# Optimization experiments

Measured on AMD Instinct MI355X. Metric: run time of the kernel, lower is better.

## Reference

```python
import jax, jax.numpy as jnp
import numpy as np

EPS = 1e-8

def _center(G):
    # Double-centering: H @ G @ H with H = I - 11^T/n, expressed as mean subtraction.
    # Identical math to the torch H-matmul version, O(n^2) instead of O(n^3).
    row = jnp.mean(G, axis=-1, keepdims=True)
    col = jnp.mean(G, axis=-2, keepdims=True)
    tot = jnp.mean(G, axis=(-2, -1), keepdims=True)
    return G - row - col + tot


def setup_inputs() -> dict:
    key = jax.random.key(0)
    k1, k2 = jax.random.split(key)
    B, L, H, M = 32, 128, 512, 512
    x = jax.random.normal(k1, (B, L, H), dtype=jnp.float32)
    # nn.Embedding.from_pretrained(torch.normal(-0.01, 0.2, (M, L*H)))
    centroid_w = jax.random.normal(k2, (M, L * H), dtype=jnp.float32) * 0.2 - 0.01
    return {"x": x, "centroid_w": centroid_w}


def reference(x, centroid_w):
    B, L, H = x.shape
    M = centroid_w.shape[0]
    cent = centroid_w.reshape(M, L, H)

    # Centered linear Grams
    Cx = _center(jnp.einsum('blh,bkh->blk', x, x))        # (B, L, L)
    Cy = _center(jnp.einsum('mlh,mkh->mlk', cent, cent))  # (M, L, L)

    # linear HSIC: sum over LxL of elementwise product -> (B, M)
    hsic = jnp.einsum('bij,mij->bm', Cx, Cy)
    vx = jnp.sqrt(jnp.sum(Cx * Cx, axis=(1, 2)))  # (B,)  sqrt(HSIC(x,x))
    vy = jnp.sqrt(jnp.sum(Cy * Cy, axis=(1, 2)))  # (M,)  sqrt(HSIC(y,y))
    cka_loss_matrix = -jnp.log(jnp.abs(hsic / (vx[:, None] * vy[None, :])) + EPS)

    idx = jnp.argmax(cka_loss_matrix, axis=-1)  # (B,)
    sel = cent[idx]                              # (B, L, H) gathered centroids

    # Second CKA pass against selected centroids; torch broadcasting makes (B, B)
    Cs = _center(jnp.einsum('blh,bkh->blk', sel, sel))  # (B, L, L)
    hsic2 = jnp.einsum('bij,cij->bc', Cx, Cs)           # (B, B)
    vs = jnp.sqrt(jnp.sum(Cs * Cs, axis=(1, 2)))        # (B,)
    cka_loss = -jnp.log(jnp.mean(jnp.abs(hsic2 / (vx[:, None] * vs[None, :]))) + EPS)

    return cka_loss, cka_loss_matrix, idx
```

## Files before the change

### kernel.cpp

```cpp
#include <hip/hip_runtime.h>
#include <math.h>

#define BB 32
#define LL 128
#define HH 512
#define MM 512
#define NM 544
#define EPSF 1e-8f
#define CPLEN 9216
#define NCH 36

typedef __attribute__((ext_vector_type(8))) short short8b;
typedef __attribute__((ext_vector_type(4))) float f32x4;

#define NWS_CP     0
#define NWS_PART   5013504
#define NWS_NSQ    5603328
#define NWS_HSIC   5603872
#define NWS_IDS    5620256

__device__ __forceinline__ float4 shflx1(float4 a) {
    float4 r;
    r.x = __shfl_xor(a.x, 1, 64);
    r.y = __shfl_xor(a.y, 1, 64);
    r.z = __shfl_xor(a.z, 1, 64);
    r.w = __shfl_xor(a.w, 1, 64);
    return r;
}

__device__ __forceinline__ unsigned pack2(unsigned lo, unsigned hi) {
    return (lo >> 16) | (hi & 0xffff0000u);
}

__device__ __forceinline__ void split3(const float4 lo, const float4 hi,
                                       uint4& p0, uint4& p1, uint4& p2) {
    float c[8] = {lo.x, lo.y, lo.z, lo.w, hi.x, hi.y, hi.z, hi.w};
    unsigned h[8], m[8], l[8];
#pragma unroll
    for (int i = 0; i < 8; ++i) {
        h[i] = __float_as_uint(c[i]) & 0xffff0000u;
        const float r1 = c[i] - __uint_as_float(h[i]);
        m[i] = __float_as_uint(r1) & 0xffff0000u;
        l[i] = __float_as_uint(r1 - __uint_as_float(m[i]));
    }
    p0 = make_uint4(pack2(h[0],h[1]), pack2(h[2],h[3]), pack2(h[4],h[5]), pack2(h[6],h[7]));
    p1 = make_uint4(pack2(m[0],m[1]), pack2(m[2],m[3]), pack2(m[4],m[5]), pack2(m[6],m[7]));
    p2 = make_uint4(pack2(l[0],l[1]), pack2(l[2],l[3]), pack2(l[4],l[5]), pack2(l[6],l[7]));
}

__device__ __forceinline__ void mfma6(f32x4& d,
                                      short8b a0, short8b a1, short8b a2,
                                      short8b b0, short8b b1, short8b b2) {
    d = __builtin_amdgcn_mfma_f32_16x16x32_bf16(a0, b0, d, 0, 0, 0);
    d = __builtin_amdgcn_mfma_f32_16x16x32_bf16(a0, b1, d, 0, 0, 0);
    d = __builtin_amdgcn_mfma_f32_16x16x32_bf16(a1, b0, d, 0, 0, 0);
    d = __builtin_amdgcn_mfma_f32_16x16x32_bf16(a1, b1, d, 0, 0, 0);
    d = __builtin_amdgcn_mfma_f32_16x16x32_bf16(a0, b2, d, 0, 0, 0);
    d = __builtin_amdgcn_mfma_f32_16x16x32_bf16(a2, b0, d, 0, 0, 0);
}

template<int W>
__device__ __forceinline__ void do_step(f32x4 (&acc)[9],
                                        const short8b (*pl)[4][128],
                                        int lane) {
    const int s = lane >> 4, lr = lane & 15;
    short8b A0[3], A1[3];
#pragma unroll
    for (int p = 0; p < 3; ++p) {
        A0[p] = pl[p][s][W * 16 + lr];
        A1[p] = pl[p][s][(7 - W) * 16 + lr];
    }
#pragma unroll
    for (int j = W; j <= 7; ++j) {
        const short8b b0 = pl[0][s][j * 16 + lr];
        const short8b b1 = pl[1][s][j * 16 + lr];
        const short8b b2 = pl[2][s][j * 16 + lr];
        mfma6(acc[j - W], A0[0], A0[1], A0[2], b0, b1, b2);
        if (j >= 7 - W)
            mfma6(acc[(8 - W) + (j - (7 - W))], A1[0], A1[1], A1[2], b0, b1, b2);
    }
}

__device__ __forceinline__ float red16(float v) {
    v += __shfl_xor(v, 1, 64);
    v += __shfl_xor(v, 2, 64);
    v += __shfl_xor(v, 4, 64);
    v += __shfl_xor(v, 8, 64);
    return v;
}

template<int W>
__device__ __forceinline__ void epi_sums(f32x4 (&acc)[9], float* Ssh128, int lane) {
    float rs0[4] = {0.f, 0.f, 0.f, 0.f};
    float rs1[4] = {0.f, 0.f, 0.f, 0.f};
#pragma unroll
    for (int j = W; j <= 7; ++j) {
        float cpj = 0.f;
        {
            const f32x4 a = acc[j - W];
#pragma unroll
            for (int q = 0; q < 4; ++q) rs0[q] += red16(a[q]);
            if (j > W) {
                float cl = a[0] + a[1] + a[2] + a[3];
                cl += __shfl_xor(cl, 16, 64);
                cl += __shfl_xor(cl, 32, 64);
                cpj += cl;
            }
        }
        if (j >= 7 - W) {
            const f32x4 a = acc[(8 - W) + (j - (7 - W))];
#pragma unroll
            for (int q = 0; q < 4; ++q) rs1[q] += red16(a[q]);
            if (j > 7 - W) {
                float cl = a[0] + a[1] + a[2] + a[3];
                cl += __shfl_xor(cl, 16, 64);
                cl += __shfl_xor(cl, 32, 64);
                cpj += cl;
            }
        }
        if (lane < 16) Ssh128[j * 16 + lane] += cpj;
    }
    if ((lane & 15) == 0) {
        const int g = lane >> 4;
#pragma unroll
        for (int q = 0; q < 4; ++q) {
            Ssh128[W * 16 + g * 4 + q]       += rs0[q];
            Ssh128[(7 - W) * 16 + g * 4 + q] += rs1[q];
        }
    }
}

template<int W>
__device__ __forceinline__ float epi_store(f32x4 (&acc)[9], const float* rmv,
                                           float gm, int lane, float* dstBase) {
    const int g = lane >> 4, c = lane & 15;
    const float R2 = 1.41421356237309505f;
    float ri0[4], ri1[4];
#pragma unroll
    for (int q = 0; q < 4; ++q) {
        ri0[q] = rmv[W * 16 + g * 4 + q];
        ri1[q] = rmv[(7 - W) * 16 + g * 4 + q];
    }
    float nsq = 0.f;
#pragma unroll
    for (int j = W; j <= 7; ++j) {
        const float rj = rmv[j * 16 + c];
        {
            f32x4 a = acc[j - W];
#pragma unroll
            for (int q = 0; q < 4; ++q) {
                a[q] += gm - ri0[q] - rj;
                if (j > W) a[q] *= R2;
                nsq = fmaf(a[q], a[q], nsq);
            }
            const int t = W * 8 - W * (W - 1) / 2 + (j - W);
            *(f32x4*)(dstBase + t * 256 + lane * 4) = a;
        }
        if (j >= 7 - W) {
            f32x4 a = acc[(8 - W) + (j - (7 - W))];
#pragma unroll
            for (int q = 0; q < 4; ++q) {
                a[q] += gm - ri1[q] - rj;
                if (j > 7 - W) a[q] *= R2;
                nsq = fmaf(a[q], a[q], nsq);
            }
            const int ti = 7 - W;
            const int t = ti * 8 - ti * (ti - 1) / 2 + (j - ti);
            *(f32x4*)(dstBase + t * 256 + lane * 4) = a;
        }
    }
    return nsq;
}

__global__ __launch_bounds__(256, 3)
void gram_sym(const float* __restrict__ x,
              const float* __restrict__ cent,
              float* __restrict__ Cp,
              float* __restrict__ normsq)
{
    __shared__ short8b planes[2][3][4][128];
    __shared__ float Ssh[4][128];
    __shared__ float rmv[128];
    __shared__ float red[256];
    __shared__ float gmsh;

    const int tid  = threadIdx.x;
    const int lane = tid & 63;
    const int wid  = tid >> 6;
    const int n    = blockIdx.x;
    const float* Amat = (n < BB) ? (x + (size_t)n * LL * HH)
                                 : (cent + (size_t)(n - BB) * LL * HH);

    const int rg  = tid >> 3;
    const int kb  = tid & 7;
    const int odd = kb & 1;
    const int s   = kb >> 1;
    const int rowA = (odd ? 64 : 0) + rg;
    const int rowB = rowA + 32;

    f32x4 acc[9];
#pragma unroll
    for (int i = 0; i < 9; ++i) acc[i] = (f32x4){0.f, 0.f, 0.f, 0.f};

    float4 v[4];
#pragma unroll
    for (int p = 0; p < 4; ++p)
        v[p] = *(const float4*)(Amat + (size_t)(rg + 32 * p) * HH + kb * 4);

    for (int t = 0; t < 16; ++t) {
        const int pb = t & 1;
        const float4 sA = odd ? v[0] : v[2];
        const float4 sB = odd ? v[1] : v[3];
        const float4 rA = shflx1(sA);
        const float4 rB = shflx1(sB);
        const float4 loA = odd ? rA : v[0];
        const float4 hiA = odd ? v[2] : rA;
        const float4 loB = odd ? rB : v[1];
        const float4 hiB = odd ? v[3] : rB;

        uint4 pA0, pA1, pA2, pB0, pB1, pB2;
        split3(loA, hiA, pA0, pA1, pA2);
        split3(loB, hiB, pB0, pB1, pB2);

        uint4* P4 = (uint4*)planes[pb];
        P4[(0 * 4 + s) * 128 + rowA] = pA0;
        P4[(1 * 4 + s) * 128 + rowA] = pA1;
        P4[(2 * 4 + s) * 128 + rowA] = pA2;
        P4[(0 * 4 + s) * 128 + rowB] = pB0;
        P4[(1 * 4 + s) * 128 + rowB] = pB1;
        P4[(2 * 4 + s) * 128 + rowB] = pB2;

        float4 vn[4];
        const int k0n = (t < 15) ? (t + 1) * 32 : 480;
#pragma unroll
        for (int p = 0; p < 4; ++p)
            vn[p] = *(const float4*)(Amat + (size_t)(rg + 32 * p) * HH + k0n + kb * 4);

        __syncthreads();

        switch (wid) {
            case 0: do_step<0>(acc, planes[pb], lane); break;
            case 1: do_step<1>(acc, planes[pb], lane); break;
            case 2: do_step<2>(acc, planes[pb], lane); break;
            default: do_step<3>(acc, planes[pb], lane); break;
        }
#pragma unroll
        for (int p = 0; p < 4; ++p) v[p] = vn[p];
    }

    Ssh[wid][lane] = 0.f;
    Ssh[wid][lane + 64] = 0.f;
    switch (wid) {
        case 0: epi_sums<0>(acc, Ssh[0], lane); break;
        case 1: epi_sums<1>(acc, Ssh[1], lane); break;
        case 2: epi_sums<2>(acc, Ssh[2], lane); break;
        default: epi_sums<3>(acc, Ssh[3], lane); break;
    }
    __syncthreads();

    float Sv = 0.f;
    if (tid < 128) {
        Sv = Ssh[0][tid] + Ssh[1][tid] + Ssh[2][tid] + Ssh[3][tid];
        rmv[tid] = Sv * (1.f / 128.f);
    }
    red[tid] = (tid < 128) ? Sv : 0.f;
    __syncthreads();
    for (int s2 = 128; s2 > 0; s2 >>= 1) {
        if (tid < s2) red[tid] += red[tid + s2];
        __syncthreads();
    }
    if (tid == 0) gmsh = red[0] * (1.f / 16384.f);
    __syncthreads();
    const float gm = gmsh;

    float nsq;
    float* dstBase = Cp + (size_t)n * CPLEN;
    switch (wid) {
        case 0: nsq = epi_store<0>(acc, rmv, gm, lane, dstBase); break;
        case 1: nsq = epi_store<1>(acc, rmv, gm, lane, dstBase); break;
        case 2: nsq = epi_store<2>(acc, rmv, gm, lane, dstBase); break;
        default: nsq = epi_store<3>(acc, rmv, gm, lane, dstBase); break;
    }
    __syncthreads();
    red[tid] = nsq;
    __syncthreads();
    for (int s2 = 128; s2 > 0; s2 >>= 1) {
        if (tid < s2) red[tid] += red[tid + s2];
        __syncthreads();
    }
    if (tid == 0) normsq[n] = red[0];
}

__global__ __launch_bounds__(256, 2)
void hsic_partial(const float* __restrict__ Cp, float* __restrict__ part)
{
    __shared__ float cx[32][260];
    __shared__ float red2[256][16];

    const int tid = threadIdx.x;
    const int bx  = blockIdx.x;
    const int mt  = bx / NCH;
    const int kc  = bx % NCH;
    const int k0  = kc * 256;

#pragma unroll
    for (int i = 0; i < 8; ++i) {
        const int idx = i * 1024 + tid * 4;
        const int b = idx >> 8, k = idx & 255;
        *(float4*)&cx[b][k] = *(const float4*)&Cp[(size_t)b * CPLEN + k0 + k];
    }
    __syncthreads();

    const int kq = tid >> 6;
    const int bg = (tid >> 3) & 7;
    const int mg = tid & 7;
    const float* cyBase = Cp + (size_t)(BB + mt * 32 + mg * 4) * CPLEN + k0 + kq * 64;

    float a[4][4];
#pragma unroll
    for (int bi = 0; bi < 4; ++bi)
#pragma unroll
        for (int mi = 0; mi < 4; ++mi) a[bi][mi] = 0.f;

    for (int kk = 0; kk < 16; ++kk) {
        float4 cy[4];
#pragma unroll
        for (int mi = 0; mi < 4; ++mi)
            cy[mi] = *(const float4*)(cyBase + (size_t)mi * CPLEN + kk * 4);
        float4 cxv[4];
#pragma unroll
        for (int bi = 0; bi < 4; ++bi)
            cxv[bi] = *(const float4*)&cx[bg + bi * 8][kq * 64 + kk * 4];
#pragma unroll
        for (int bi = 0; bi < 4; ++bi)
#pragma unroll
            for (int mi = 0; mi < 4; ++mi) {
                a[bi][mi] = fmaf(cxv[bi].x, cy[mi].x, a[bi][mi]);
                a[bi][mi] = fmaf(cxv[bi].y, cy[mi].y, a[bi][mi]);
                a[bi][mi] = fmaf(cxv[bi].z, cy[mi].z, a[bi][mi]);
                a[bi][mi] = fmaf(cxv[bi].w, cy[mi].w, a[bi][mi]);
            }
    }

#pragma unroll
    for (int e = 0; e < 16; ++e) red2[tid][e] = a[e >> 2][e & 3];
    __syncthreads();
    if (tid < 64) {
#pragma unroll
        for (int e = 0; e < 16; ++e) {
            const float s = red2[tid][e] + red2[tid + 64][e] +
                            red2[tid + 128][e] + red2[tid + 192][e];
            const int bi = e >> 2, mi = e & 3;
            const int b = ((tid >> 3) & 7) + bi * 8;
            const int m = mt * 32 + (tid & 7) * 4 + mi;
            part[((size_t)kc * 32 + b) * 512 + m] = s;
        }
    }
}

__global__ __launch_bounds__(256)
void combine_loss(const float* __restrict__ part,
                  const float* __restrict__ normsq,
                  float* __restrict__ hsic,
                  int* __restrict__ ids,
                  float* __restrict__ out)
{
    __shared__ float rv[256];
    __shared__ int   ri[256];
    const int b = blockIdx.x;
    const int tid = threadIdx.x;
    const float vx = sqrtf(normsq[b]);

    float best = -INFINITY; int bm = 0;
    for (int m = tid; m < MM; m += 256) {
        float s = 0.f;
        for (int kc = 0; kc < NCH; ++kc)
            s += part[((size_t)kc * 32 + b) * 512 + m];
        hsic[b * MM + m] = s;
        const float vy = sqrtf(normsq[BB + m]);
        const float loss = -logf(fabsf(s) / (vx * vy) + EPSF);
        out[1 + b * MM + m] = loss;
        if (loss > best) { best = loss; bm = m; }
    }
    rv[tid] = best; ri[tid] = bm;
    __syncthreads();
    for (int s2 = 128; s2 > 0; s2 >>= 1) {
        if (tid < s2) {
            if (rv[tid + s2] > rv[tid] ||
                (rv[tid + s2] == rv[tid] && ri[tid + s2] < ri[tid])) {
                rv[tid] = rv[tid + s2]; ri[tid] = ri[tid + s2];
            }
        }
        __syncthreads();
    }
    if (tid == 0) { ids[b] = ri[0]; out[1 + BB * MM + b] = (float)ri[0]; }
}

__global__ __launch_bounds__(1024)
void scalar_loss(const float* __restrict__ hsic,
                 const float* __restrict__ normsq,
                 const int* __restrict__ ids,
                 float* __restrict__ out)
{
    __shared__ float red[1024];
    const int tid = threadIdx.x;
    const int b = tid >> 5, c = tid & 31;
    const int m = ids[c];
    red[tid] = fabsf(hsic[b * MM + m]) /
               (sqrtf(normsq[b]) * sqrtf(normsq[BB + m]));
    __syncthreads();
    for (int s = 512; s > 0; s >>= 1) {
        if (tid < s) red[tid] += red[tid + s];
        __syncthreads();
    }
    if (tid == 0) out[0] = -logf(red[0] * (1.f / 1024.f) + EPSF);
}

extern "C" void kernel_launch(void* const* d_in, const int* in_sizes, int n_in,
                              void* d_out, int out_size, void* d_ws, size_t ws_size,
                              hipStream_t stream) {
    const float* x    = (const float*)d_in[0];
    const float* cent = (const float*)d_in[1];
    float* out = (float*)d_out;
    float* ws  = (float*)d_ws;

    float* Cp     = ws + NWS_CP;
    float* part   = ws + NWS_PART;
    float* normsq = ws + NWS_NSQ;
    float* hsic   = ws + NWS_HSIC;
    int*   ids    = (int*)(ws + NWS_IDS);

    gram_sym<<<NM, 256, 0, stream>>>(x, cent, Cp, normsq);
    hsic_partial<<<16 * NCH, 256, 0, stream>>>(Cp, part);
    combine_loss<<<BB, 256, 0, stream>>>(part, normsq, hsic, ids, out);
    scalar_loss<<<1, 1024, 0, stream>>>(hsic, normsq, ids, out);
}
```

Measured before the change: 102.5 us.

## Switch Gram kernel to 32x32 MFMA tiles with 4x4 upper-triangle tiling

```diff
diff --git a/kernel.cpp b/kernel.cpp
--- a/kernel.cpp
+++ b/kernel.cpp
@@ -7,26 +7,18 @@
 #define MM 512
 #define NM 544
 #define EPSF 1e-8f
-#define CPLEN 9216
-#define NCH 36
+#define CPLEN 10240
+#define NCH 40
 
 typedef __attribute__((ext_vector_type(8))) short short8b;
 typedef __attribute__((ext_vector_type(4))) float f32x4;
-
-#define NWS_CP     0
-#define NWS_PART   5013504
-#define NWS_NSQ    5603328
-#define NWS_HSIC   5603872
-#define NWS_IDS    5620256
-
-__device__ __forceinline__ float4 shflx1(float4 a) {
-    float4 r;
-    r.x = __shfl_xor(a.x, 1, 64);
-    r.y = __shfl_xor(a.y, 1, 64);
-    r.z = __shfl_xor(a.z, 1, 64);
-    r.w = __shfl_xor(a.w, 1, 64);
-    return r;
-}
+typedef __attribute__((ext_vector_type(16))) float f32x16;
+
+#define NWS_CP    0
+#define NWS_PART  5570560
+#define NWS_NSQ   6225920
+#define NWS_HSIC  6226464
+#define NWS_IDS   6242848
 
 __device__ __forceinline__ unsigned pack2(unsigned lo, unsigned hi) {
     return (lo >> 16) | (hi & 0xffff0000u);
@@ -48,137 +40,84 @@
     p2 = make_uint4(pack2(l[0],l[1]), pack2(l[2],l[3]), pack2(l[4],l[5]), pack2(l[6],l[7]));
 }
 
-__device__ __forceinline__ void mfma6(f32x4& d,
-                                      short8b a0, short8b a1, short8b a2,
-                                      short8b b0, short8b b1, short8b b2) {
-    d = __builtin_amdgcn_mfma_f32_16x16x32_bf16(a0, b0, d, 0, 0, 0);
-    d = __builtin_amdgcn_mfma_f32_16x16x32_bf16(a0, b1, d, 0, 0, 0);
-    d = __builtin_amdgcn_mfma_f32_16x16x32_bf16(a1, b0, d, 0, 0, 0);
-    d = __builtin_amdgcn_mfma_f32_16x16x32_bf16(a1, b1, d, 0, 0, 0);
-    d = __builtin_amdgcn_mfma_f32_16x16x32_bf16(a0, b2, d, 0, 0, 0);
-    d = __builtin_amdgcn_mfma_f32_16x16x32_bf16(a2, b0, d, 0, 0, 0);
-}
-
-template<int W>
-__device__ __forceinline__ void do_step(f32x4 (&acc)[9],
-                                        const short8b (*pl)[4][128],
-                                        int lane) {
-    const int s = lane >> 4, lr = lane & 15;
-    short8b A0[3], A1[3];
+__device__ __forceinline__ f32x16 mfma6(f32x16 d, const short8b a[3], const short8b b[3]) {
+    d = __builtin_amdgcn_mfma_f32_32x32x16_bf16(a[0], b[0], d, 0, 0, 0);
+    d = __builtin_amdgcn_mfma_f32_32x32x16_bf16(a[0], b[1], d, 0, 0, 0);
+    d = __builtin_amdgcn_mfma_f32_32x32x16_bf16(a[1], b[0], d, 0, 0, 0);
+    d = __builtin_amdgcn_mfma_f32_32x32x16_bf16(a[1], b[1], d, 0, 0, 0);
+    d = __builtin_amdgcn_mfma_f32_32x32x16_bf16(a[0], b[2], d, 0, 0, 0);
+    d = __builtin_amdgcn_mfma_f32_32x32x16_bf16(a[2], b[0], d, 0, 0, 0);
+    return d;
+}
+
+__device__ __forceinline__ void ldstrip(const uint4* P, int strip, int lane, short8b f[3]) {
+    const int s = lane >> 5;
+    const int r = strip * 32 + (lane & 31);
 #pragma unroll
     for (int p = 0; p < 3; ++p) {
-        A0[p] = pl[p][s][W * 16 + lr];
-        A1[p] = pl[p][s][(7 - W) * 16 + lr];
-    }
-#pragma unroll
-    for (int j = W; j <= 7; ++j) {
-        const short8b b0 = pl[0][s][j * 16 + lr];
-        const short8b b1 = pl[1][s][j * 16 + lr];
-        const short8b b2 = pl[2][s][j * 16 + lr];
-        mfma6(acc[j - W], A0[0], A0[1], A0[2], b0, b1, b2);
-        if (j >= 7 - W)
-            mfma6(acc[(8 - W) + (j - (7 - W))], A1[0], A1[1], A1[2], b0, b1, b2);
-    }
-}
-
-__device__ __forceinline__ float red16(float v) {
-    v += __shfl_xor(v, 1, 64);
-    v += __shfl_xor(v, 2, 64);
-    v += __shfl_xor(v, 4, 64);
-    v += __shfl_xor(v, 8, 64);
-    return v;
-}
-
-template<int W>
-__device__ __forceinline__ void epi_sums(f32x4 (&acc)[9], float* Ssh128, int lane) {
-    float rs0[4] = {0.f, 0.f, 0.f, 0.f};
-    float rs1[4] = {0.f, 0.f, 0.f, 0.f};
-#pragma unroll
-    for (int j = W; j <= 7; ++j) {
-        float cpj = 0.f;
-        {
-            const f32x4 a = acc[j - W];
-#pragma unroll
-            for (int q = 0; q < 4; ++q) rs0[q] += red16(a[q]);
-            if (j > W) {
-                float cl = a[0] + a[1] + a[2] + a[3];
-                cl += __shfl_xor(cl, 16, 64);
-                cl += __shfl_xor(cl, 32, 64);
-                cpj += cl;
-            }
+        uint4 u = P[(p * 2 + s) * 128 + r];
+        f[p] = *(const short8b*)&u;
+    }
+}
+
+__device__ __forceinline__ void tile_sums(f32x16 a, float* S, int i, int j,
+                                          bool offd, int lane) {
+    const int hi = lane >> 5;
+    float rs[16];
+#pragma unroll
+    for (int q = 0; q < 16; ++q) {
+        float s = a[q];
+        s += __shfl_xor(s, 1, 64);
+        s += __shfl_xor(s, 2, 64);
+        s += __shfl_xor(s, 4, 64);
+        s += __shfl_xor(s, 8, 64);
+        s += __shfl_xor(s, 16, 64);
+        rs[q] = s;
+    }
+    if ((lane & 31) == 0) {
+#pragma unroll
+        for (int q = 0; q < 16; ++q)
+            S[i * 32 + (q & 3) + 8 * (q >> 2) + 4 * hi] += rs[q];
+    }
+    if (offd) {
+        float cs = 0.f;
+#pragma unroll
+        for (int q = 0; q < 16; ++q) cs += a[q];
+        cs += __shfl_xor(cs, 32, 64);
+        if (lane < 32) S[j * 32 + lane] += cs;
+    }
+}
+
+__device__ __forceinline__ float tile_fin(f32x16 a, const float* rmv, float gm,
+                                          bool offd, int i, int j,
+                                          float* dst, int lane) {
+    const int hi = lane >> 5, col = lane & 31;
+    const float cj = rmv[j * 32 + col];
+    const float sc = offd ? 1.41421356237309505f : 1.f;
+    float nsq = 0.f;
+#pragma unroll
+    for (int c = 0; c < 4; ++c) {
+        const float4 ri = *(const float4*)&rmv[i * 32 + c * 8 + hi * 4];
+        const float riq[4] = {ri.x, ri.y, ri.z, ri.w};
+        f32x4 o;
+#pragma unroll
+        for (int q = 0; q < 4; ++q) {
+            float vq = (a[c * 4 + q] + gm - riq[q] - cj) * sc;
+            nsq = fmaf(vq, vq, nsq);
+            o[q] = vq;
         }
-        if (j >= 7 - W) {
-            const f32x4 a = acc[(8 - W) + (j - (7 - W))];
-#pragma unroll
-            for (int q = 0; q < 4; ++q) rs1[q] += red16(a[q]);
-            if (j > 7 - W) {
-                float cl = a[0] + a[1] + a[2] + a[3];
-                cl += __shfl_xor(cl, 16, 64);
-                cl += __shfl_xor(cl, 32, 64);
-                cpj += cl;
-            }
-        }
-        if (lane < 16) Ssh128[j * 16 + lane] += cpj;
-    }
-    if ((lane & 15) == 0) {
-        const int g = lane >> 4;
-#pragma unroll
-        for (int q = 0; q < 4; ++q) {
-            Ssh128[W * 16 + g * 4 + q]       += rs0[q];
-            Ssh128[(7 - W) * 16 + g * 4 + q] += rs1[q];
-        }
-    }
-}
-
-template<int W>
-__device__ __forceinline__ float epi_store(f32x4 (&acc)[9], const float* rmv,
-                                           float gm, int lane, float* dstBase) {
-    const int g = lane >> 4, c = lane & 15;
-    const float R2 = 1.41421356237309505f;
-    float ri0[4], ri1[4];
-#pragma unroll
-    for (int q = 0; q < 4; ++q) {
-        ri0[q] = rmv[W * 16 + g * 4 + q];
-        ri1[q] = rmv[(7 - W) * 16 + g * 4 + q];
-    }
-    float nsq = 0.f;
-#pragma unroll
-    for (int j = W; j <= 7; ++j) {
-        const float rj = rmv[j * 16 + c];
-        {
-            f32x4 a = acc[j - W];
-#pragma unroll
-            for (int q = 0; q < 4; ++q) {
-                a[q] += gm - ri0[q] - rj;
-                if (j > W) a[q] *= R2;
-                nsq = fmaf(a[q], a[q], nsq);
-            }
-            const int t = W * 8 - W * (W - 1) / 2 + (j - W);
-            *(f32x4*)(dstBase + t * 256 + lane * 4) = a;
-        }
-        if (j >= 7 - W) {
-            f32x4 a = acc[(8 - W) + (j - (7 - W))];
-#pragma unroll
-            for (int q = 0; q < 4; ++q) {
-                a[q] += gm - ri1[q] - rj;
-                if (j > 7 - W) a[q] *= R2;
-                nsq = fmaf(a[q], a[q], nsq);
-            }
-            const int ti = 7 - W;
-            const int t = ti * 8 - ti * (ti - 1) / 2 + (j - ti);
-            *(f32x4*)(dstBase + t * 256 + lane * 4) = a;
-        }
+        *(f32x4*)(dst + (c * 2 + hi) * 128 + col * 4) = o;
     }
     return nsq;
 }
 
-__global__ __launch_bounds__(256, 3)
-void gram_sym(const float* __restrict__ x,
-              const float* __restrict__ cent,
-              float* __restrict__ Cp,
-              float* __restrict__ normsq)
+__global__ __launch_bounds__(256, 4)
+void gram_sym2(const float* __restrict__ x,
+               const float* __restrict__ cent,
+               float* __restrict__ Cp,
+               float* __restrict__ normsq)
 {
-    __shared__ short8b planes[2][3][4][128];
+    __shared__ uint4 planes[2][3][2][128];
     __shared__ float Ssh[4][128];
     __shared__ float rmv[128];
     __shared__ float red[256];
@@ -191,70 +130,70 @@
     const float* Amat = (n < BB) ? (x + (size_t)n * LL * HH)
                                  : (cent + (size_t)(n - BB) * LL * HH);
 
-    const int rg  = tid >> 3;
-    const int kb  = tid & 7;
-    const int odd = kb & 1;
-    const int s   = kb >> 1;
-    const int rowA = (odd ? 64 : 0) + rg;
-    const int rowB = rowA + 32;
-
-    f32x4 acc[9];
-#pragma unroll
-    for (int i = 0; i < 9; ++i) acc[i] = (f32x4){0.f, 0.f, 0.f, 0.f};
-
-    float4 v[4];
-#pragma unroll
-    for (int p = 0; p < 4; ++p)
-        v[p] = *(const float4*)(Amat + (size_t)(rg + 32 * p) * HH + kb * 4);
-
-    for (int t = 0; t < 16; ++t) {
+    const int srow  = tid >> 1;
+    const int shalf = tid & 1;
+
+    f32x16 a0, a1, a2;
+#pragma unroll
+    for (int q = 0; q < 16; ++q) { a0[q] = 0.f; a1[q] = 0.f; a2[q] = 0.f; }
+
+    float4 v0 = *(const float4*)(Amat + (size_t)srow * HH + shalf * 8);
+    float4 v1 = *(const float4*)(Amat + (size_t)srow * HH + shalf * 8 + 4);
+
+    for (int t = 0; t < 32; ++t) {
         const int pb = t & 1;
-        const float4 sA = odd ? v[0] : v[2];
-        const float4 sB = odd ? v[1] : v[3];
-        const float4 rA = shflx1(sA);
-        const float4 rB = shflx1(sB);
-        const float4 loA = odd ? rA : v[0];
-        const float4 hiA = odd ? v[2] : rA;
-        const float4 loB = odd ? rB : v[1];
-        const float4 hiB = odd ? v[3] : rB;
-
-        uint4 pA0, pA1, pA2, pB0, pB1, pB2;
-        split3(loA, hiA, pA0, pA1, pA2);
-        split3(loB, hiB, pB0, pB1, pB2);
-
-        uint4* P4 = (uint4*)planes[pb];
-        P4[(0 * 4 + s) * 128 + rowA] = pA0;
-        P4[(1 * 4 + s) * 128 + rowA] = pA1;
-        P4[(2 * 4 + s) * 128 + rowA] = pA2;
-        P4[(0 * 4 + s) * 128 + rowB] = pB0;
-        P4[(1 * 4 + s) * 128 + rowB] = pB1;
-        P4[(2 * 4 + s) * 128 + rowB] = pB2;
-
-        float4 vn[4];
-        const int k0n = (t < 15) ? (t + 1) * 32 : 480;
-#pragma unroll
-        for (int p = 0; p < 4; ++p)
-            vn[p] = *(const float4*)(Amat + (size_t)(rg + 32 * p) * HH + k0n + kb * 4);
-
-        __syncthreads();
-
-        switch (wid) {
-            case 0: do_step<0>(acc, planes[pb], lane); break;
-            case 1: do_step<1>(acc, planes[pb], lane); break;
-            case 2: do_step<2>(acc, planes[pb], lane); break;
-            default: do_step<3>(acc, planes[pb], lane); break;
+        uint4 p0, p1, p2;
+        split3(v0, v1, p0, p1, p2);
+        uint4* P = &planes[pb][0][0][0];
+        const int wbase = shalf * 128 + srow;
+        P[0 * 256 + wbase] = p0;
+        P[1 * 256 + wbase] = p1;
+        P[2 * 256 + wbase] = p2;
+
+        const int kn = (t < 31) ? (t + 1) * 16 : 496;
+        v0 = *(const float4*)(Amat + (size_t)srow * HH + kn + shalf * 8);
+        v1 = *(const float4*)(Amat + (size_t)srow * HH + kn + shalf * 8 + 4);
+
+        __syncthreads();
+
+        const uint4* Pr = &planes[pb][0][0][0];
+        short8b fa[3], fb[3];
+        if (wid == 0) {
+            ldstrip(Pr, 3, lane, fb);
+            ldstrip(Pr, 0, lane, fa); a0 = mfma6(a0, fa, fb);
+            ldstrip(Pr, 1, lane, fa); a1 = mfma6(a1, fa, fb);
+            ldstrip(Pr, 2, lane, fa); a2 = mfma6(a2, fa, fb);
+        } else if (wid == 1) {
+            ldstrip(Pr, 3, lane, fa); a0 = mfma6(a0, fa, fa);
+            ldstrip(Pr, 2, lane, fb);
+            ldstrip(Pr, 0, lane, fa); a1 = mfma6(a1, fa, fb);
+            ldstrip(Pr, 1, lane, fa); a2 = mfma6(a2, fa, fb);
+        } else if (wid == 2) {
+            ldstrip(Pr, 2, lane, fa); a0 = mfma6(a0, fa, fa);
+            ldstrip(Pr, 0, lane, fa);
+            ldstrip(Pr, 1, lane, fb); a1 = mfma6(a1, fa, fb);
+        } else {
+            ldstrip(Pr, 0, lane, fa); a0 = mfma6(a0, fa, fa);
+            ldstrip(Pr, 1, lane, fa); a1 = mfma6(a1, fa, fa);
         }
-#pragma unroll
-        for (int p = 0; p < 4; ++p) v[p] = vn[p];
     }
 
     Ssh[wid][lane] = 0.f;
     Ssh[wid][lane + 64] = 0.f;
-    switch (wid) {
-        case 0: epi_sums<0>(acc, Ssh[0], lane); break;
-        case 1: epi_sums<1>(acc, Ssh[1], lane); break;
-        case 2: epi_sums<2>(acc, Ssh[2], lane); break;
-        default: epi_sums<3>(acc, Ssh[3], lane); break;
+    if (wid == 0) {
+        tile_sums(a0, Ssh[0], 0, 3, true, lane);
+        tile_sums(a1, Ssh[0], 1, 3, true, lane);
+        tile_sums(a2, Ssh[0], 2, 3, true, lane);
+    } else if (wid == 1) {
+        tile_sums(a0, Ssh[1], 3, 3, false, lane);
+        tile_sums(a1, Ssh[1], 0, 2, true, lane);
+        tile_sums(a2, Ssh[1], 1, 2, true, lane);
+    } else if (wid == 2) {
+        tile_sums(a0, Ssh[2], 2, 2, false, lane);
+        tile_sums(a1, Ssh[2], 0, 1, true, lane);
+    } else {
+        tile_sums(a0, Ssh[3], 0, 0, false, lane);
+        tile_sums(a1, Ssh[3], 1, 1, false, lane);
     }
     __syncthreads();
 
@@ -273,13 +212,22 @@
     __syncthreads();
     const float gm = gmsh;
 
-    float nsq;
-    float* dstBase = Cp + (size_t)n * CPLEN;
-    switch (wid) {
-        case 0: nsq = epi_store<0>(acc, rmv, gm, lane, dstBase); break;
-        case 1: nsq = epi_store<1>(acc, rmv, gm, lane, dstBase); break;
-        case 2: nsq = epi_store<2>(acc, rmv, gm, lane, dstBase); break;
-        default: nsq = epi_store<3>(acc, rmv, gm, lane, dstBase); break;
+    float nsq = 0.f;
+    float* dst = Cp + (size_t)n * CPLEN;
+    if (wid == 0) {
+        nsq += tile_fin(a0, rmv, gm, true, 0, 3, dst + 3 * 1024, lane);
+        nsq += tile_fin(a1, rmv, gm, true, 1, 3, dst + 6 * 1024, lane);
+        nsq += tile_fin(a2, rmv, gm, true, 2, 3, dst + 8 * 1024, lane);
+    } else if (wid == 1) {
+        nsq += tile_fin(a0, rmv, gm, false, 3, 3, dst + 9 * 1024, lane);
+        nsq += tile_fin(a1, rmv, gm, true, 0, 2, dst + 2 * 1024, lane);
+        nsq += tile_fin(a2, rmv, gm, true, 1, 2, dst + 5 * 1024, lane);
+    } else if (wid == 2) {
+        nsq += tile_fin(a0, rmv, gm, false, 2, 2, dst + 7 * 1024, lane);
+        nsq += tile_fin(a1, rmv, gm, true, 0, 1, dst + 1 * 1024, lane);
+    } else {
+        nsq += tile_fin(a0, rmv, gm, false, 0, 0, dst + 0 * 1024, lane);
+        nsq += tile_fin(a1, rmv, gm, false, 1, 1, dst + 4 * 1024, lane);
     }
     __syncthreads();
     red[tid] = nsq;
@@ -430,7 +378,7 @@
     float* hsic   = ws + NWS_HSIC;
     int*   ids    = (int*)(ws + NWS_IDS);
 
-    gram_sym<<<NM, 256, 0, stream>>>(x, cent, Cp, normsq);
+    gram_sym2<<<NM, 256, 0, stream>>>(x, cent, Cp, normsq);
     hsic_partial<<<16 * NCH, 256, 0, stream>>>(Cp, part);
     combine_loss<<<BB, 256, 0, stream>>>(part, normsq, hsic, ids, out);
     scalar_loss<<<1, 1024, 0, stream>>>(hsic, normsq, ids, out);
```

After: 89.42 us. -12.7%, faster.
